# Kernel tuning notes

Hardware: AMD Instinct MI355X
Metric: run time of the kernel (lower is better)

Reference implementation:

```python
import jax, jax.numpy as jnp
import numpy as np
import math

EMBED = 256
NH = 8      # num_heads
NP = 4      # num_points
HD = EMBED // NH  # head_dim = 32
BS = 8
NQ = 8192
HH = 128
WW = 128


def setup_inputs() -> dict:
    key = jax.random.key(0)
    ks = jax.random.split(key, 12)
    query = jax.random.normal(ks[0], (BS, NQ, EMBED), jnp.float32)
    reference_points = jax.random.uniform(ks[1], (BS, NQ, 2), dtype=jnp.float32)
    value = jax.random.normal(ks[2], (BS, HH * WW, EMBED), jnp.float32)
    # sampling_offsets: torch init uses zero weight + structured bias (rose pattern);
    # use small random weight so the math path is exercised, keep the structured bias.
    w_off = 0.001 * jax.random.normal(ks[3], (EMBED, NH * NP * 2), jnp.float32)
    thetas = np.arange(NH, dtype=np.float32) * (2.0 * math.pi / NH)
    grid = np.stack([np.cos(thetas), np.sin(thetas)], -1)          # [NH, 2]
    grid = np.tile(grid[:, None, :], (1, NP, 1)) * np.arange(1, NP + 1, dtype=np.float32)[None, :, None]
    b_off = jnp.asarray(grid.reshape(-1), jnp.float32)              # [NH*NP*2]
    w_attn = 0.01 * jax.random.normal(ks[4], (EMBED, NH * NP), jnp.float32)
    b_attn = jnp.zeros((NH * NP,), jnp.float32)
    xav = 1.0 / math.sqrt(EMBED)
    w_val = xav * jax.random.normal(ks[5], (EMBED, EMBED), jnp.float32)
    b_val = jnp.zeros((EMBED,), jnp.float32)
    w_out = xav * jax.random.normal(ks[6], (EMBED, EMBED), jnp.float32)
    b_out = jnp.zeros((EMBED,), jnp.float32)
    return {"query": query, "reference_points": reference_points, "value": value,
            "w_off": w_off, "b_off": b_off, "w_attn": w_attn, "b_attn": b_attn,
            "w_val": w_val, "b_val": b_val, "w_out": w_out, "b_out": b_out,
            "H": HH, "W": WW}


def _deform_attn(query, reference_points, value, w_off, b_off, w_attn, b_attn,
                 w_val, b_val, w_out, b_out, H, W):
    bs, nq, _ = query.shape
    # value projection -> [bs, nh, H*W, hd]
    v = (value @ w_val + b_val).reshape(bs, H * W, NH, HD).transpose(0, 2, 1, 3)
    # offsets and attention weights
    off = (query @ w_off + b_off).reshape(bs, nq, NH, NP, 2)
    attn = jax.nn.softmax((query @ w_attn + b_attn).reshape(bs, nq, NH, NP), axis=-1)
    norm = jnp.array([W, H], dtype=query.dtype)
    loc = reference_points[:, :, None, None, :] + off / norm       # [bs,nq,nh,np,2] in [0,1]
    # grid_sample, align_corners=False: pixel = loc*size - 0.5  (x <-> W, y <-> H)
    px = (loc[..., 0] * W - 0.5).transpose(0, 2, 1, 3).reshape(bs, NH, nq * NP)
    py = (loc[..., 1] * H - 0.5).transpose(0, 2, 1, 3).reshape(bs, NH, nq * NP)
    x0 = jnp.floor(px); y0 = jnp.floor(py)
    wx = px - x0; wy = py - y0
    x0i = x0.astype(jnp.int32); y0i = y0.astype(jnp.int32)

    def gather(xi, yi):
        # padding_mode='zeros': out-of-range corners contribute 0
        mask = ((xi >= 0) & (xi < W) & (yi >= 0) & (yi < H)).astype(v.dtype)
        idx = jnp.clip(yi, 0, H - 1) * W + jnp.clip(xi, 0, W - 1)   # [bs,nh,K]
        g = jnp.take_along_axis(v, idx[..., None], axis=2)          # [bs,nh,K,hd]
        return g * mask[..., None]

    samp = (((1 - wx) * (1 - wy))[..., None] * gather(x0i, y0i)
            + (wx * (1 - wy))[..., None] * gather(x0i + 1, y0i)
            + ((1 - wx) * wy)[..., None] * gather(x0i, y0i + 1)
            + (wx * wy)[..., None] * gather(x0i + 1, y0i + 1))      # [bs,nh,nq*np,hd]
    samp = samp.reshape(bs, NH, nq, NP, HD)
    aw = attn.transpose(0, 2, 1, 3)                                 # [bs,nh,nq,np]
    out = jnp.einsum('bhqpd,bhqp->bqhd', samp, aw).reshape(bs, nq, EMBED)
    return out @ w_out + b_out


def reference(query, reference_points, value, w_off, b_off, w_attn, b_attn,
              w_val, b_val, w_out, b_out, H, W):
    return _deform_attn(query, reference_points, value, w_off, b_off, w_attn, b_attn,
                        w_val, b_val, w_out, b_out, H, W)
```

## Files before the change

kernel.cpp:

```cpp
#include <hip/hip_runtime.h>
#include <stdint.h>

#define NQ 8192
#define BSZ 8
#define NH 8
#define NP 4
#define HD 32
#define EMBED 256
#define IMG 128
#define NPIX (IMG*IMG)

typedef __attribute__((ext_vector_type(8))) short short8v;
typedef __attribute__((ext_vector_type(4))) float f32x4;

static __device__ __forceinline__ float bf2f(uint32_t u) {
    union { uint32_t i; float f; } x; x.i = u << 16; return x.f;
}
static __device__ __forceinline__ uint16_t f2bf(float f) {
    union { float f; uint32_t i; } x; x.f = f;
    uint32_t r = x.i + 0x7fffu + ((x.i >> 16) & 1u);
    return (uint16_t)(r >> 16);
}
static __device__ __forceinline__ uint32_t cvtpk(float lo, float hi) {
    uint32_t r;
    asm("v_cvt_pk_bf16_f32 %0, %1, %2" : "=v"(r) : "v"(lo), "v"(hi));
    return r;
}
static __device__ __forceinline__ void gload_lds16(const void* g, void* l) {
    __builtin_amdgcn_global_load_lds(
        (const __attribute__((address_space(1))) unsigned int*)g,
        (__attribute__((address_space(3))) unsigned int*)l, 16, 0, 0);
}

#define WAITV(n) asm volatile("s_waitcnt vmcnt(" #n ")" ::: "memory")
#define WAITLGKM() do { asm volatile("s_waitcnt lgkmcnt(0)" ::: "memory"); \
                        __builtin_amdgcn_sched_barrier(0); } while (0)
#define BARRIER() do { __builtin_amdgcn_s_barrier(); \
                       __builtin_amdgcn_sched_barrier(0); } while (0)

static __device__ __forceinline__ void waitv_n(int n) {
    switch (n) {
        case 0: WAITV(0); break;  case 1: WAITV(1); break;
        case 2: WAITV(2); break;  case 3: WAITV(3); break;
        case 4: WAITV(4); break;  default: WAITV(5); break;
    }
}

__global__ void pack_w(const float* __restrict__ w_val, const float* __restrict__ w_out,
                       const float* __restrict__ w_off, const float* __restrict__ w_attn,
                       uint16_t* __restrict__ wTval, uint16_t* __restrict__ wTout,
                       uint16_t* __restrict__ wTcat) {
    int k = blockIdx.x;
    int n = threadIdx.x;
    wTval[n * 256 + k] = f2bf(w_val[k * 256 + n]);
    wTout[n * 256 + k] = f2bf(w_out[k * 256 + n]);
    if (n < 64)       wTcat[n * 256 + k]        = f2bf(w_off[k * 64 + n]);
    else if (n < 96)  wTcat[n * 256 + k]        = f2bf(w_attn[k * 32 + (n - 64)]);
}

template<bool A_F32, bool OUT_F32, bool PLANE, int STRIPES>
__global__ __launch_bounds__(512, 2)
void gemm_pk(const void* __restrict__ Ap, const uint16_t* __restrict__ BT,
             void* __restrict__ Cp, const float* __restrict__ bias) {
    constexpr int T = STRIPES * 4;
    __shared__ char SMEM[131072 + (PLANE ? 32768 : 0)];
    char* ring = SMEM;
    const int tid = threadIdx.x, w = tid >> 6, l = tid & 63;
    const int stripe0 = blockIdx.x * STRIPES;

    auto grow0 = [&](int t) { return (stripe0 + (t >> 2)) * 64 + (t & 3) * 16; };

    auto loadA = [&](int t, float4 (&fb)[2]) {
        const char* src = (const char*)Ap + (size_t)(grow0(t) + (tid & 15)) * 1024
                          + (tid >> 4) * 32;
        fb[0] = ((const float4*)src)[0];
        fb[1] = ((const float4*)src)[1];
    };
    auto writeA = [&](int t, const float4 (&fb)[2]) {
        uint4 pk;
        pk.x = cvtpk(fb[0].x, fb[0].y); pk.y = cvtpk(fb[0].z, fb[0].w);
        pk.z = cvtpk(fb[1].x, fb[1].y); pk.w = cvtpk(fb[1].z, fb[1].w);
        *(uint4*)(ring + (t & 15) * 8192 + tid * 16) = pk;
    };
    auto stageA_lds = [&](int t) {
        const char* src = (const char*)Ap + (size_t)(grow0(t) + (l & 15)) * 512
                          + (l >> 4) * 16 + w * 64;
        gload_lds16(src, ring + (t & 15) * 8192 + w * 1024);
    };

    float4 fbuf[2][2];
    if constexpr (A_F32) { loadA(0, fbuf[0]); loadA(1, fbuf[1]); }

#pragma unroll
    for (int c = 0; c < 16; ++c) {
        int loff = c * 8192 + tid * 16;
        int row = loff >> 9, x = loff & 511;
        const char* src = (const char*)BT + (size_t)row * 512 + (x ^ ((row & 7) << 4));
        gload_lds16(src, SMEM + c * 8192 + w * 1024);
    }
    WAITV(0);
    BARRIER();
    short8v breg[2][8];
#pragma unroll
    for (int n = 0; n < 2; ++n) {
        int col = w * 32 + n * 16 + (l & 15);
        const char* base = SMEM + col * 512;
        const int sz = (col & 7) << 4;
#pragma unroll
        for (int k = 0; k < 8; ++k)
            breg[n][k] = *(const short8v*)(base + ((k * 64 + (l >> 4) * 16) ^ sz));
    }
    WAITLGKM();
    BARRIER();
    if constexpr (A_F32) {
        writeA(0, fbuf[0]);
    } else {
#pragma unroll
        for (int t = 0; t < 6; ++t) stageA_lds(t);
    }

    for (int st = 0; st < STRIPES; ++st) {
        f32x4 acc[4][2] = {};
#pragma unroll
        for (int s = 0; s < 4; ++s) {
            const int t = st * 4 + s;
            if constexpr (A_F32) {
                if (t + 2 < T) loadA(t + 2, fbuf[s & 1]);
                if (t + 1 < T) writeA(t + 1, fbuf[(s + 1) & 1]);
                WAITLGKM();
                BARRIER();
            } else {
                const int rem = T - 1 - t;
                waitv_n(rem < 5 ? rem : 5);
                BARRIER();
                if (t + 6 < T) stageA_lds(t + 6);
            }
            const char* abase = ring + (t & 15) * 8192 + l * 16;
            short8v a[8];
#pragma unroll
            for (int k = 0; k < 8; ++k)
                a[k] = *(const short8v*)(abase + k * 1024);
#pragma unroll
            for (int k = 0; k < 8; ++k)
#pragma unroll
                for (int n = 0; n < 2; ++n)
                    acc[s][n] = __builtin_amdgcn_mfma_f32_16x16x32_bf16(a[k], breg[n][k], acc[s][n], 0, 0, 0);
        }

        const int gr0 = (stripe0 + st) * 64;
        if constexpr (PLANE) {
            char* Cs = SMEM + 131072;
#pragma unroll
            for (int s = 0; s < 4; ++s)
#pragma unroll
                for (int n = 0; n < 2; ++n) {
                    int lcol = w * 32 + n * 16 + (l & 15);
                    float bv = bias[lcol];
#pragma unroll
                    for (int r = 0; r < 4; ++r) {
                        int lrow = s * 16 + (l >> 4) * 4 + r;
                        *(uint16_t*)(Cs + ((lrow * 512 + lcol * 2) ^ ((lrow & 7) << 4)))
                            = f2bf(acc[s][n][r] + bv);
                    }
                }
            WAITLGKM();
            BARRIER();
            const int b_ = gr0 >> 14, pix0 = gr0 & 16383;
            char* pb = (char*)Cp + (((size_t)(b_ * 8 + w)) << 20) + (size_t)pix0 * 64;
#pragma unroll
            for (int i = 0; i < 4; ++i) {
                int fb = i * 1024 + l * 16;
                int lrow = fb >> 6, x = w * 64 + (fb & 63);
                uint4 d = *(const uint4*)(Cs + ((lrow * 512 + x) ^ ((lrow & 7) << 4)));
                *(uint4*)(pb + (size_t)lrow * 64 + (fb & 63)) = d;
            }
            WAITLGKM();
            BARRIER();
        } else {
#pragma unroll
            for (int s = 0; s < 4; ++s)
#pragma unroll
                for (int n = 0; n < 2; ++n) {
                    int col = w * 32 + n * 16 + (l & 15);
                    float bv = bias[col];
#pragma unroll
                    for (int r = 0; r < 4; ++r) {
                        int gr = gr0 + s * 16 + (l >> 4) * 4 + r;
                        float val = acc[s][n][r] + bv;
                        if constexpr (OUT_F32)
                            ((float*)Cp)[(size_t)gr * 256 + col] = val;
                        else
                            ((uint16_t*)Cp)[(size_t)gr * 256 + col] = f2bf(val);
                    }
                }
        }
    }
}

__global__ __launch_bounds__(256, 2)
void proj_kernel(const float* __restrict__ Q, const uint16_t* __restrict__ WTcat,
                 const float* __restrict__ b_off, const float* __restrict__ b_attn,
                 const float* __restrict__ refp,
                 float* __restrict__ locs, float* __restrict__ attnw) {
    __shared__ uint16_t Bs[96 * 256];
    __shared__ uint16_t As[64 * 256];
    const int tid = threadIdx.x, w = tid >> 6, l = tid & 63;
    const int blk = blockIdx.x;

#pragma unroll
    for (int c = 0; c < 12; ++c) {
        int loff = (w * 12 + c) * 1024;
        int lofl = loff + l * 16;
        int row = lofl >> 9, colb = lofl & 511;
        const char* src = (const char*)WTcat + (size_t)row * 512 + (colb ^ ((row & 7) << 4));
        gload_lds16(src, (char*)Bs + loff);
    }
#pragma unroll
    for (int c = 0; c < 8; ++c) {
        int loff = tid * 16 + c * 4096;
        int row = loff >> 9, colb = loff & 511;
        const float* src = Q + (size_t)(blk * 64 + row) * 256 + (colb >> 1);
        float4 f0 = *(const float4*)src;
        float4 f1 = *(const float4*)(src + 4);
        uint4 pk;
        pk.x = (uint32_t)f2bf(f0.x) | ((uint32_t)f2bf(f0.y) << 16);
        pk.y = (uint32_t)f2bf(f0.z) | ((uint32_t)f2bf(f0.w) << 16);
        pk.z = (uint32_t)f2bf(f1.x) | ((uint32_t)f2bf(f1.y) << 16);
        pk.w = (uint32_t)f2bf(f1.z) | ((uint32_t)f2bf(f1.w) << 16);
        *(uint4*)((char*)As + row * 512 + (colb ^ ((row & 7) << 4))) = pk;
    }
    __syncthreads();

    f32x4 acc[6] = {};
    const int arow = w * 16 + (l & 15);
#pragma unroll
    for (int ks = 0; ks < 8; ++ks) {
        const int kb = ks * 64 + (l >> 4) * 16;
        short8v a = *(const short8v*)((const char*)As + arow * 512 + (kb ^ ((arow & 7) << 4)));
#pragma unroll
        for (int n = 0; n < 6; ++n) {
            int col = n * 16 + (l & 15);
            short8v b = *(const short8v*)((const char*)Bs + col * 512 + (kb ^ ((col & 7) << 4)));
            acc[n] = __builtin_amdgcn_mfma_f32_16x16x32_bf16(a, b, acc[n], 0, 0, 0);
        }
    }
    __syncthreads();
    float* scores = (float*)As;
#pragma unroll
    for (int n = 0; n < 6; ++n)
#pragma unroll
        for (int r = 0; r < 4; ++r)
            scores[(w * 16 + (l >> 4) * 4 + r) * 96 + n * 16 + (l & 15)] = acc[n][r];
    __syncthreads();

    for (int it = tid; it < 512; it += 256) {
        int row = it >> 3, h = it & 7;
        int gq = blk * 64 + row;
        int b = gq >> 13, q = gq & 8191;
        size_t itemH = ((size_t)(b * 8 + h) << 13) | q;
        float s0 = scores[row * 96 + 64 + h * 4 + 0] + b_attn[h * 4 + 0];
        float s1 = scores[row * 96 + 64 + h * 4 + 1] + b_attn[h * 4 + 1];
        float s2 = scores[row * 96 + 64 + h * 4 + 2] + b_attn[h * 4 + 2];
        float s3 = scores[row * 96 + 64 + h * 4 + 3] + b_attn[h * 4 + 3];
        float mx = fmaxf(fmaxf(s0, s1), fmaxf(s2, s3));
        float e0 = __expf(s0 - mx), e1 = __expf(s1 - mx);
        float e2 = __expf(s2 - mx), e3 = __expf(s3 - mx);
        float inv = 1.0f / (e0 + e1 + e2 + e3);
        float rx = refp[gq * 2 + 0] * 128.0f - 0.5f;
        float ry = refp[gq * 2 + 1] * 128.0f - 0.5f;
        float ew[4] = { e0, e1, e2, e3 };
#pragma unroll
        for (int p = 0; p < 4; ++p) {
            float ox = scores[row * 96 + h * 8 + p * 2 + 0] + b_off[h * 8 + p * 2 + 0];
            float oy = scores[row * 96 + h * 8 + p * 2 + 1] + b_off[h * 8 + p * 2 + 1];
            locs[itemH * 8 + p * 2 + 0] = rx + ox;
            locs[itemH * 8 + p * 2 + 1] = ry + oy;
            attnw[itemH * 4 + p] = ew[p] * inv;
        }
    }
}

__global__ __launch_bounds__(256)
void sample_kernel(const uint16_t* __restrict__ v, const float* __restrict__ locs,
                   const float* __restrict__ attnw, uint16_t* __restrict__ oatt) {
    const int bid = blockIdx.x;
    const int h = bid & 7;
    const int rest = bid >> 3;
    const int b = rest >> 7;
    const int chunk = rest & 127;
    const int qloc = threadIdx.x >> 2;
    const int dg = threadIdx.x & 3;
    const int q = chunk * 64 + qloc;
    const size_t itemH = ((size_t)(b * 8 + h) << 13) | q;
    const char* plane = (const char*)v + ((size_t)(b * 8 + h) << 20);

    float4 l01 = ((const float4*)locs)[itemH * 2 + 0];
    float4 l23 = ((const float4*)locs)[itemH * 2 + 1];
    float4 aw4 = ((const float4*)attnw)[itemH];
    float pxs[4] = { l01.x, l01.z, l23.x, l23.z };
    float pys[4] = { l01.y, l01.w, l23.y, l23.w };
    float aws[4] = { aw4.x, aw4.y, aw4.z, aw4.w };

    float acc[8] = {};
#pragma unroll
    for (int p = 0; p < 4; ++p) {
        float px = pxs[p], py = pys[p], aw = aws[p];
        float fx = floorf(px), fy = floorf(py);
        float wx = px - fx, wy = py - fy;
        int x0 = (int)fx, y0 = (int)fy;
#pragma unroll
        for (int cy = 0; cy < 2; ++cy) {
            int yy = y0 + cy;
            float wyv = cy ? wy : 1.f - wy;
            bool yok = (unsigned)yy < (unsigned)IMG;
            int yc = min(max(yy, 0), IMG - 1);
#pragma unroll
            for (int cx = 0; cx < 2; ++cx) {
                int xx = x0 + cx;
                bool ok = yok && ((unsigned)xx < (unsigned)IMG);
                int xc = min(max(xx, 0), IMG - 1);
                float wgt = ok ? aw * (cx ? wx : 1.f - wx) * wyv : 0.f;
                const uint4 u = *(const uint4*)(plane + ((size_t)(yc * IMG + xc) << 6) + dg * 16);
                acc[0] += wgt * bf2f(u.x & 0xffffu);
                acc[1] += wgt * bf2f(u.x >> 16);
                acc[2] += wgt * bf2f(u.y & 0xffffu);
                acc[3] += wgt * bf2f(u.y >> 16);
                acc[4] += wgt * bf2f(u.z & 0xffffu);
                acc[5] += wgt * bf2f(u.z >> 16);
                acc[6] += wgt * bf2f(u.w & 0xffffu);
                acc[7] += wgt * bf2f(u.w >> 16);
            }
        }
    }
    const size_t bq = (size_t)b * NQ + q;
    uint4 out;
    out.x = (uint32_t)f2bf(acc[0]) | ((uint32_t)f2bf(acc[1]) << 16);
    out.y = (uint32_t)f2bf(acc[2]) | ((uint32_t)f2bf(acc[3]) << 16);
    out.z = (uint32_t)f2bf(acc[4]) | ((uint32_t)f2bf(acc[5]) << 16);
    out.w = (uint32_t)f2bf(acc[6]) | ((uint32_t)f2bf(acc[7]) << 16);
    *(uint4*)((char*)oatt + (bq * 256 + h * 32 + dg * 8) * 2) = out;
}

extern "C" void kernel_launch(void* const* d_in, const int* in_sizes, int n_in,
                              void* d_out, int out_size, void* d_ws, size_t ws_size,
                              hipStream_t stream) {
    const float* query  = (const float*)d_in[0];
    const float* refp   = (const float*)d_in[1];
    const float* value  = (const float*)d_in[2];
    const float* w_off  = (const float*)d_in[3];
    const float* b_off  = (const float*)d_in[4];
    const float* w_attn = (const float*)d_in[5];
    const float* b_attn = (const float*)d_in[6];
    const float* w_val  = (const float*)d_in[7];
    const float* b_val  = (const float*)d_in[8];
    const float* w_out  = (const float*)d_in[9];
    const float* b_out  = (const float*)d_in[10];

    char* ws = (char*)d_ws;
    uint16_t* v     = (uint16_t*)(ws);
    uint16_t* oatt  = (uint16_t*)(ws + 67108864);
    float*    locs  = (float*)(ws + 100663296);
    float*    attnw = (float*)(ws + 117440512);
    uint16_t* wTval = (uint16_t*)(ws + 125829120);
    uint16_t* wTout = (uint16_t*)(ws + 125960192);
    uint16_t* wTcat = (uint16_t*)(ws + 126091264);

    pack_w<<<256, 256, 0, stream>>>(w_val, w_out, w_off, w_attn, wTval, wTout, wTcat);
    gemm_pk<true, false, true, 8><<<256, 512, 0, stream>>>(value, wTval, v, b_val);
    proj_kernel<<<1024, 256, 0, stream>>>(query, wTcat, b_off, b_attn, refp, locs, attnw);
    sample_kernel<<<8192, 256, 0, stream>>>(v, locs, attnw, oatt);
    gemm_pk<false, true, false, 4><<<256, 512, 0, stream>>>(oatt, wTout, (float*)d_out, b_out);
}
```

Measured before the change: 142.9 us.

## Load B fragments directly from global, shrink LDS ring, double GEMM grid

The GEMM kernel no longer stages the full transposed weight matrix through LDS. Each lane now reads its B fragments straight from global memory into registers, which removes a 128KB LDS staging pass and two barriers. The A ring buffer shrinks to 4 or 8 slots, cutting LDS per block so more blocks can be resident per CU. Both GEMM launches halve stripes per block and double the grid to 512 blocks. The trade-off is uncoalesced global reads of B per wave and more repeated weight fetches across blocks.

```diff
diff --git a/kernel.cpp b/kernel.cpp
--- a/kernel.cpp
+++ b/kernel.cpp
@@ -63,7 +63,8 @@
 void gemm_pk(const void* __restrict__ Ap, const uint16_t* __restrict__ BT,
              void* __restrict__ Cp, const float* __restrict__ bias) {
     constexpr int T = STRIPES * 4;
-    __shared__ char SMEM[131072 + (PLANE ? 32768 : 0)];
+    constexpr int SLOTS = A_F32 ? 4 : 8;
+    __shared__ char SMEM[SLOTS * 8192 + (PLANE ? 32768 : 0)];
     char* ring = SMEM;
     const int tid = threadIdx.x, w = tid >> 6, l = tid & 63;
     const int stripe0 = blockIdx.x * STRIPES;
@@ -80,38 +81,27 @@
         uint4 pk;
         pk.x = cvtpk(fb[0].x, fb[0].y); pk.y = cvtpk(fb[0].z, fb[0].w);
         pk.z = cvtpk(fb[1].x, fb[1].y); pk.w = cvtpk(fb[1].z, fb[1].w);
-        *(uint4*)(ring + (t & 15) * 8192 + tid * 16) = pk;
+        *(uint4*)(ring + (t & (SLOTS - 1)) * 8192 + tid * 16) = pk;
     };
     auto stageA_lds = [&](int t) {
         const char* src = (const char*)Ap + (size_t)(grow0(t) + (l & 15)) * 512
-                          + (l >> 4) * 16 + w * 64;
-        gload_lds16(src, ring + (t & 15) * 8192 + w * 1024);
+                          + w * 64 + (l >> 4) * 16;
+        gload_lds16(src, ring + (t & (SLOTS - 1)) * 8192 + w * 1024);
     };
 
     float4 fbuf[2][2];
     if constexpr (A_F32) { loadA(0, fbuf[0]); loadA(1, fbuf[1]); }
 
-#pragma unroll
-    for (int c = 0; c < 16; ++c) {
-        int loff = c * 8192 + tid * 16;
-        int row = loff >> 9, x = loff & 511;
-        const char* src = (const char*)BT + (size_t)row * 512 + (x ^ ((row & 7) << 4));
-        gload_lds16(src, SMEM + c * 8192 + w * 1024);
-    }
-    WAITV(0);
-    BARRIER();
     short8v breg[2][8];
 #pragma unroll
     for (int n = 0; n < 2; ++n) {
-        int col = w * 32 + n * 16 + (l & 15);
-        const char* base = SMEM + col * 512;
-        const int sz = (col & 7) << 4;
+        const char* bb = (const char*)BT + (size_t)(w * 32 + n * 16 + (l & 15)) * 512
+                         + (l >> 4) * 16;
 #pragma unroll
         for (int k = 0; k < 8; ++k)
-            breg[n][k] = *(const short8v*)(base + ((k * 64 + (l >> 4) * 16) ^ sz));
-    }
-    WAITLGKM();
-    BARRIER();
+            breg[n][k] = *(const short8v*)(bb + k * 64);
+    }
+
     if constexpr (A_F32) {
         writeA(0, fbuf[0]);
     } else {
@@ -135,7 +125,7 @@
                 BARRIER();
                 if (t + 6 < T) stageA_lds(t + 6);
             }
-            const char* abase = ring + (t & 15) * 8192 + l * 16;
+            const char* abase = ring + (t & (SLOTS - 1)) * 8192 + l * 16;
             short8v a[8];
 #pragma unroll
             for (int k = 0; k < 8; ++k)
@@ -149,7 +139,7 @@
 
         const int gr0 = (stripe0 + st) * 64;
         if constexpr (PLANE) {
-            char* Cs = SMEM + 131072;
+            char* Cs = SMEM + SLOTS * 8192;
 #pragma unroll
             for (int s = 0; s < 4; ++s)
 #pragma unroll
@@ -366,8 +356,8 @@
     uint16_t* wTcat = (uint16_t*)(ws + 126091264);
 
     pack_w<<<256, 256, 0, stream>>>(w_val, w_out, w_off, w_attn, wTval, wTout, wTcat);
-    gemm_pk<true, false, true, 8><<<256, 512, 0, stream>>>(value, wTval, v, b_val);
+    gemm_pk<true, false, true, 4><<<512, 512, 0, stream>>>(value, wTval, v, b_val);
     proj_kernel<<<1024, 256, 0, stream>>>(query, wTcat, b_off, b_attn, refp, locs, attnw);
     sample_kernel<<<8192, 256, 0, stream>>>(v, locs, attnw, oatt);
-    gemm_pk<false, true, false, 4><<<256, 512, 0, stream>>>(oatt, wTout, (float*)d_out, b_out);
-}
+    gemm_pk<false, true, false, 2><<<512, 512, 0, stream>>>(oatt, wTout, (float*)d_out, b_out);
+}
```

New measurement: 153.8 us. +7.6%, slower.

## Pre-convert value tensor to bf16 and use async LDS loads in value GEMM

Applied to the files above, without the earlier changes.

Adds a standalone kernel that converts the fp32 value tensor to bf16 in workspace. The value projection GEMM then uses the same direct global-to-LDS async staging path as the output GEMM, and the in-register fp32 load/convert path is removed. This aims to replace the register-staged, barrier-heavy A pipeline with deeper asynchronous prefetch. In exchange it adds an extra full pass over the value tensor, raising total memory traffic, and needs a larger workspace.

```diff
diff --git a/kernel.cpp b/kernel.cpp
--- a/kernel.cpp
+++ b/kernel.cpp
@@ -58,10 +58,24 @@
     else if (n < 96)  wTcat[n * 256 + k]        = f2bf(w_attn[k * 32 + (n - 64)]);
 }
 
-template<bool A_F32, bool OUT_F32, bool PLANE, int STRIPES>
+__global__ __launch_bounds__(256)
+void cvt_kernel(const float* __restrict__ in, uint16_t* __restrict__ out, int n8) {
+    int i = blockIdx.x * 256 + threadIdx.x;
+    const int stride = gridDim.x * 256;
+    for (; i < n8; i += stride) {
+        const float4* p = (const float4*)in + (size_t)i * 2;
+        float4 a = p[0], b = p[1];
+        uint4 o;
+        o.x = cvtpk(a.x, a.y); o.y = cvtpk(a.z, a.w);
+        o.z = cvtpk(b.x, b.y); o.w = cvtpk(b.z, b.w);
+        ((uint4*)out)[i] = o;
+    }
+}
+
+template<bool OUT_F32, bool PLANE, int STRIPES>
 __global__ __launch_bounds__(512, 2)
-void gemm_pk(const void* __restrict__ Ap, const uint16_t* __restrict__ BT,
-             void* __restrict__ Cp, const float* __restrict__ bias) {
+void gemm_bf16(const uint16_t* __restrict__ Ap, const uint16_t* __restrict__ BT,
+               void* __restrict__ Cp, const float* __restrict__ bias) {
     constexpr int T = STRIPES * 4;
     __shared__ char SMEM[131072 + (PLANE ? 32768 : 0)];
     char* ring = SMEM;
@@ -69,27 +83,11 @@
     const int stripe0 = blockIdx.x * STRIPES;
 
     auto grow0 = [&](int t) { return (stripe0 + (t >> 2)) * 64 + (t & 3) * 16; };
-
-    auto loadA = [&](int t, float4 (&fb)[2]) {
-        const char* src = (const char*)Ap + (size_t)(grow0(t) + (tid & 15)) * 1024
-                          + (tid >> 4) * 32;
-        fb[0] = ((const float4*)src)[0];
-        fb[1] = ((const float4*)src)[1];
-    };
-    auto writeA = [&](int t, const float4 (&fb)[2]) {
-        uint4 pk;
-        pk.x = cvtpk(fb[0].x, fb[0].y); pk.y = cvtpk(fb[0].z, fb[0].w);
-        pk.z = cvtpk(fb[1].x, fb[1].y); pk.w = cvtpk(fb[1].z, fb[1].w);
-        *(uint4*)(ring + (t & 15) * 8192 + tid * 16) = pk;
-    };
-    auto stageA_lds = [&](int t) {
+    auto stageA = [&](int t) {
         const char* src = (const char*)Ap + (size_t)(grow0(t) + (l & 15)) * 512
-                          + (l >> 4) * 16 + w * 64;
+                          + w * 64 + (l >> 4) * 16;
         gload_lds16(src, ring + (t & 15) * 8192 + w * 1024);
     };
-
-    float4 fbuf[2][2];
-    if constexpr (A_F32) { loadA(0, fbuf[0]); loadA(1, fbuf[1]); }
 
 #pragma unroll
     for (int c = 0; c < 16; ++c) {
@@ -112,29 +110,18 @@
     }
     WAITLGKM();
     BARRIER();
-    if constexpr (A_F32) {
-        writeA(0, fbuf[0]);
-    } else {
-#pragma unroll
-        for (int t = 0; t < 6; ++t) stageA_lds(t);
-    }
+#pragma unroll
+    for (int t = 0; t < 6; ++t) stageA(t);
 
     for (int st = 0; st < STRIPES; ++st) {
         f32x4 acc[4][2] = {};
 #pragma unroll
         for (int s = 0; s < 4; ++s) {
             const int t = st * 4 + s;
-            if constexpr (A_F32) {
-                if (t + 2 < T) loadA(t + 2, fbuf[s & 1]);
-                if (t + 1 < T) writeA(t + 1, fbuf[(s + 1) & 1]);
-                WAITLGKM();
-                BARRIER();
-            } else {
-                const int rem = T - 1 - t;
-                waitv_n(rem < 5 ? rem : 5);
-                BARRIER();
-                if (t + 6 < T) stageA_lds(t + 6);
-            }
+            const int rem = T - 1 - t;
+            waitv_n(rem < 5 ? rem : 5);
+            BARRIER();
+            if (t + 6 < T) stageA(t + 6);
             const char* abase = ring + (t & 15) * 8192 + l * 16;
             short8v a[8];
 #pragma unroll
@@ -358,16 +345,18 @@
 
     char* ws = (char*)d_ws;
     uint16_t* v     = (uint16_t*)(ws);
-    uint16_t* oatt  = (uint16_t*)(ws + 67108864);
-    float*    locs  = (float*)(ws + 100663296);
-    float*    attnw = (float*)(ws + 117440512);
-    uint16_t* wTval = (uint16_t*)(ws + 125829120);
-    uint16_t* wTout = (uint16_t*)(ws + 125960192);
-    uint16_t* wTcat = (uint16_t*)(ws + 126091264);
+    uint16_t* oatt  = (uint16_t*)(ws + (64u << 20));
+    float*    locs  = (float*)(ws + (96u << 20));
+    float*    attnw = (float*)(ws + (112u << 20));
+    uint16_t* wTval = (uint16_t*)(ws + (120u << 20));
+    uint16_t* wTout = (uint16_t*)(ws + (120u << 20) + 131072);
+    uint16_t* wTcat = (uint16_t*)(ws + (120u << 20) + 262144);
+    uint16_t* abf16 = (uint16_t*)(ws + (192u << 20));
 
     pack_w<<<256, 256, 0, stream>>>(w_val, w_out, w_off, w_attn, wTval, wTout, wTcat);
-    gemm_pk<true, false, true, 8><<<256, 512, 0, stream>>>(value, wTval, v, b_val);
+    cvt_kernel<<<4096, 256, 0, stream>>>(value, abf16, 131072 * 256 / 8);
+    gemm_bf16<false, true, 8><<<256, 512, 0, stream>>>(abf16, wTval, v, b_val);
     proj_kernel<<<1024, 256, 0, stream>>>(query, wTcat, b_off, b_attn, refp, locs, attnw);
     sample_kernel<<<8192, 256, 0, stream>>>(v, locs, attnw, oatt);
-    gemm_pk<false, true, false, 4><<<256, 512, 0, stream>>>(oatt, wTout, (float*)d_out, b_out);
-}
+    gemm_bf16<true, false, 4><<<256, 512, 0, stream>>>(oatt, wTout, (float*)d_out, b_out);
+}
```

New measurement: 165.0 us. 1.15x slower.
